# Optimization experiments

Hardware: AMD Instinct MI355X
Metric: run time of the kernel (lower is better)

The kernel has to match this reference:

```python
import jax, jax.numpy as jnp
import numpy as np

BN_EPS = 1e-5


def ball_query(pos, radius, k):
    """PointNet++-style ball query: for each point, the first k point indices
    (in index order) whose distance < radius; shorter lists are padded with the
    first valid index (self is always valid since dist=0). pos: (b,n,3).
    Returns idx: (b,n,k) int32."""
    b, n, _ = pos.shape
    sq = jnp.sum(pos * pos, axis=-1)                       # (b,n)
    d2 = sq[:, :, None] + sq[:, None, :] - 2.0 * jnp.einsum('bnc,bmc->bnm', pos, pos)
    mask = d2 < radius * radius                            # (b,n,n)
    cand = jnp.where(mask, jnp.arange(n, dtype=jnp.int32)[None, None, :], jnp.int32(n))
    # smallest-k indices in ascending order == first-k valid in index order
    neg_top, _ = jax.lax.top_k(-cand, k)                   # (b,n,k)
    idx = -neg_top
    first = idx[..., :1]
    idx = jnp.where(idx == n, first, idx)                  # pad with first neighbor
    return idx


def reference(pos, x, w1, gamma, beta, w2, b2, radius, k):
    pos = jax.lax.stop_gradient(pos)
    idx = ball_query(pos, radius, k)                       # (b,n,k)
    grouped = jax.vmap(lambda p, i: p[i])(pos, idx)        # (b,n,k,3)
    rel = grouped - pos[:, :, None, :]                     # center-subtract
    # 1x1 conv (3->3, no bias)
    h = jnp.einsum('bnkc,dc->bnkd', rel, w1)
    # BatchNorm2d (training-mode batch stats over b,k,n per channel)
    mean = jnp.mean(h, axis=(0, 1, 2))
    var = jnp.mean((h - mean) ** 2, axis=(0, 1, 2))
    h = (h - mean) * jax.lax.rsqrt(var + BN_EPS) * gamma + beta
    h = jax.nn.relu(h)
    # 1x1 conv (3->out_channel) + bias
    pe = jnp.einsum('bnkd,ed->bnke', h, w2) + b2           # (b,n,k,C)
    pe = jnp.max(pe, axis=2)                               # max over k neighbors
    return x + pe


def setup_inputs() -> dict:
    key = jax.random.key(0)
    ks = jax.random.split(key, 5)
    b, n, c, kk = 2, 8192, 64, 32
    pos = jax.random.uniform(ks[0], (b, n, 3), dtype=jnp.float32)
    x = jax.random.normal(ks[1], (b, n, c), dtype=jnp.float32)
    w1 = jax.random.normal(ks[2], (3, 3), dtype=jnp.float32) * 0.5
    gamma = jnp.ones((3,), dtype=jnp.float32)
    beta = jnp.zeros((3,), dtype=jnp.float32)
    w2 = jax.random.normal(ks[3], (c, 3), dtype=jnp.float32) * 0.5
    b2 = jnp.zeros((c,), dtype=jnp.float32)
    radius = jnp.float32(0.1)
    return {"pos": pos, "x": x, "w1": w1, "gamma": gamma, "beta": beta,
            "w2": w2, "b2": b2, "radius": radius, "k": kk}
```

## Files before the change

### kernel.cpp

```cpp
#include <hip/hip_runtime.h>
#include <math.h>

#define NPTS   8192
#define NBATCH 2
#define NQ     (NPTS * NBATCH)
#define KNB    32
#define CFEAT  64
#define BN_EPS 1e-5f

#define MAXC     1000
#define CSTR     1024
#define CAP_HIT  128

#define QBK2  4
#define NBLK2 (NQ / QBK2)

#define QBK3  16
#define NBLK3 (NQ / QBK3)

#define WS_H     0
#define WS_PART  (NQ * 3 * KNB)
#define WS_STATS (WS_PART + 6 * NBLK2)
#define WS_CS    (WS_STATS + 8)
#define WS_BIN   (WS_CS + 2 * CSTR)

__device__ __forceinline__ int grid_from_r(double rd) {
    int G = (int)(1.0 / rd);
    if (G < 1) G = 1;
    while (G > 1 && 1.0 / (double)G < rd) --G;
    if (G > 10) G = 10;
    return G;
}

__device__ __forceinline__ int mbcnt64(unsigned long long m) {
    return (int)__builtin_amdgcn_mbcnt_hi((unsigned)(m >> 32),
             __builtin_amdgcn_mbcnt_lo((unsigned)m, 0u));
}

__global__ __launch_bounds__(256) void kA_bin(
    const float* __restrict__ pos, const float* __restrict__ radius,
    float* __restrict__ ws)
{
    __shared__ int hist[MAXC];
    __shared__ int offs[MAXC];
    __shared__ int cur[MAXC];
    __shared__ int wtot[4];

    const int tid = threadIdx.x, lane = tid & 63, wave = tid >> 6;
    const int batch = blockIdx.x;
    const float* bpos = pos + (size_t)batch * NPTS * 3;
    const double rd = (double)radius[0];
    const int G = grid_from_r(rd);
    const float Gf = (float)G;
    const int NC = G * G * G;

    for (int c = tid; c < NC; c += 256) hist[c] = 0;
    __syncthreads();
    for (int p = tid; p < NPTS; p += 256) {
        float x = bpos[p * 3], y = bpos[p * 3 + 1], z = bpos[p * 3 + 2];
        int cx = min((int)(x * Gf), G - 1);
        int cy = min((int)(y * Gf), G - 1);
        int cz = min((int)(z * Gf), G - 1);
        atomicAdd(&hist[(cz * G + cy) * G + cx], 1);
    }
    __syncthreads();

    const int c0 = tid * 4;
    int h0 = (c0 + 0 < NC) ? hist[c0 + 0] : 0;
    int h1 = (c0 + 1 < NC) ? hist[c0 + 1] : 0;
    int h2 = (c0 + 2 < NC) ? hist[c0 + 2] : 0;
    int h3 = (c0 + 3 < NC) ? hist[c0 + 3] : 0;
    const int tsum = h0 + h1 + h2 + h3;
    int incl = tsum;
#pragma unroll
    for (int off = 1; off < 64; off <<= 1) {
        int v = __shfl_up(incl, off);
        if (lane >= off) incl += v;
    }
    if (lane == 63) wtot[wave] = incl;
    __syncthreads();
    int wbase = 0;
#pragma unroll
    for (int w = 0; w < 4; ++w) wbase += (w < wave) ? wtot[w] : 0;
    int base = wbase + incl - tsum;
    if (c0 + 0 < NC) { offs[c0 + 0] = base; cur[c0 + 0] = base; base += h0; }
    if (c0 + 1 < NC) { offs[c0 + 1] = base; cur[c0 + 1] = base; base += h1; }
    if (c0 + 2 < NC) { offs[c0 + 2] = base; cur[c0 + 2] = base; base += h2; }
    if (c0 + 3 < NC) { offs[c0 + 3] = base; cur[c0 + 3] = base; base += h3; }
    __syncthreads();

    int* cs = (int*)ws + WS_CS + batch * CSTR;
    for (int c = tid; c <= NC; c += 256) cs[c] = (c < NC) ? offs[c] : NPTS;

    float4* bin = (float4*)(ws + WS_BIN) + (size_t)batch * NPTS;
    for (int p = tid; p < NPTS; p += 256) {
        float x = bpos[p * 3], y = bpos[p * 3 + 1], z = bpos[p * 3 + 2];
        int cx = min((int)(x * Gf), G - 1);
        int cy = min((int)(y * Gf), G - 1);
        int cz = min((int)(z * Gf), G - 1);
        int slot = atomicAdd(&cur[(cz * G + cy) * G + cx], 1);
        bin[slot] = make_float4(x, y, z, __int_as_float(p));
    }
}

__global__ __launch_bounds__(256) void k2_query(
    const float* __restrict__ pos, const float* __restrict__ w1,
    const float* __restrict__ radius, float* __restrict__ ws)
{
    __shared__ int   hitl[QBK2][CAP_HIT];
    __shared__ int   seli[QBK2][KNB];
    __shared__ float sred[QBK2][6];

    const int tid = threadIdx.x, lane = tid & 63, wave = tid >> 6;
    const int qbase = blockIdx.x * QBK2;
    const int batch = qbase / NPTS;
    const float* bpos = pos + (size_t)batch * NPTS * 3;
    const double rd  = (double)radius[0];
    const double r2d = rd * rd;
    const int G = grid_from_r(rd);
    const float Gf = (float)G;
    const int* cs = (const int*)ws + WS_CS + batch * CSTR;
    const float4* bin = (const float4*)(ws + WS_BIN) + (size_t)batch * NPTS;

    const int qg = qbase + wave;
    const int ql = qg - batch * NPTS;
    const float qx = bpos[ql * 3], qy = bpos[ql * 3 + 1], qz = bpos[ql * 3 + 2];
    const double qxd = (double)qx, qyd = (double)qy, qzd = (double)qz;
    const double qsd = fma(qzd, qzd, fma(qyd, qyd, qxd * qxd));
    const int cx = min((int)(qx * Gf), G - 1);
    const int cy = min((int)(qy * Gf), G - 1);
    const int cz = min((int)(qz * Gf), G - 1);
    const int cx0 = max(cx - 1, 0), cx1 = min(cx + 1, G - 1);

    int hc = 0;
#pragma unroll
    for (int r = 0; r < 9; ++r) {
        const int ny = cy + (r % 3) - 1;
        const int nz = cz + (r / 3) - 1;
        if (ny < 0 || ny >= G || nz < 0 || nz >= G) continue;
        const int cb = (nz * G + ny) * G;
        const int s0 = cs[cb + cx0];
        const int s1 = cs[cb + cx1 + 1];
        for (int b0 = s0; b0 < s1; b0 += 64) {
            const int ss = b0 + lane;
            const bool act = ss < s1;
            float4 P = bin[act ? ss : s0];
            double xj = (double)P.x, yj = (double)P.y, zj = (double)P.z;
            double sqj = fma(zj, zj, fma(yj, yj, xj * xj));
            double dot = fma(zj, qzd, fma(yj, qyd, xj * qxd));
            double dd  = (qsd + sqj) - 2.0 * dot;
            bool in = act && (dd < r2d);
            unsigned long long bal = __ballot(in);
            if (in) {
                int p2 = hc + mbcnt64(bal);
                if (p2 < CAP_HIT) hitl[wave][p2] = __float_as_int(P.w);
            }
            hc += (int)__popcll(bal);
        }
    }
    if (hc > CAP_HIT) hc = CAP_HIT;

    if (hc <= KNB) {
        int v = (lane < hc) ? hitl[wave][lane] : 0x7FFFFFFF;
        int mn = v;
#pragma unroll
        for (int off = 32; off; off >>= 1) mn = min(mn, __shfl_xor(mn, off));
        if (lane < KNB) seli[wave][lane] = (lane < hc) ? v : mn;
    } else {
        int a = (lane < hc) ? hitl[wave][lane] : 0x7FFFFFFF;
        int b = (64 + lane < hc) ? hitl[wave][64 + lane] : 0x7FFFFFFF;
        int lo = 0, hi = NPTS - 1;
        while (lo < hi) {
            int mid = (lo + hi) >> 1;
            int c1 = (int)__popcll(__ballot(a <= mid)) +
                     (int)__popcll(__ballot(b <= mid));
            if (c1 >= KNB) hi = mid; else lo = mid + 1;
        }
        const int t = lo;
        unsigned long long ba = __ballot(a <= t);
        unsigned long long bb = __ballot(b <= t);
        int na = (int)__popcll(ba);
        if (a <= t) seli[wave][mbcnt64(ba)] = a;
        if (b <= t) seli[wave][na + mbcnt64(bb)] = b;
    }

    float w1r[9];
#pragma unroll
    for (int i = 0; i < 9; ++i) w1r[i] = w1[i];

    float ls0 = 0.f, ls1 = 0.f, ls2 = 0.f;
    float lq0 = 0.f, lq1 = 0.f, lq2 = 0.f;
    if (lane < KNB) {
        int j = seli[wave][lane];
        const float* pj = bpos + (size_t)j * 3;
        float rx = __fsub_rn(pj[0], qx);
        float ry = __fsub_rn(pj[1], qy);
        float rz = __fsub_rn(pj[2], qz);
        float h0 = fmaf(rz, w1r[2], fmaf(ry, w1r[1], __fmul_rn(rx, w1r[0])));
        float h1 = fmaf(rz, w1r[5], fmaf(ry, w1r[4], __fmul_rn(rx, w1r[3])));
        float h2 = fmaf(rz, w1r[8], fmaf(ry, w1r[7], __fmul_rn(rx, w1r[6])));
        float* hout = ws + WS_H + (size_t)qg * 3 * KNB;
        hout[0 * KNB + lane] = h0;
        hout[1 * KNB + lane] = h1;
        hout[2 * KNB + lane] = h2;
        ls0 = h0; ls1 = h1; ls2 = h2;
        lq0 = h0 * h0; lq1 = h1 * h1; lq2 = h2 * h2;
    }

#pragma unroll
    for (int m = 1; m < 64; m <<= 1) {
        ls0 += __shfl_xor(ls0, m); ls1 += __shfl_xor(ls1, m); ls2 += __shfl_xor(ls2, m);
        lq0 += __shfl_xor(lq0, m); lq1 += __shfl_xor(lq1, m); lq2 += __shfl_xor(lq2, m);
    }
    if (lane == 0) {
        sred[wave][0] = ls0; sred[wave][1] = ls1; sred[wave][2] = ls2;
        sred[wave][3] = lq0; sred[wave][4] = lq1; sred[wave][5] = lq2;
    }
    __syncthreads();
    if (tid < 6) {
        float s = sred[0][tid] + sred[1][tid] + sred[2][tid] + sred[3][tid];
        ws[WS_PART + tid * NBLK2 + blockIdx.x] = s;
    }
}

__global__ __launch_bounds__(1024) void k2b_stats(float* __restrict__ ws)
{
    __shared__ float wred[16][6];
    const int tid = threadIdx.x, lane = tid & 63, wave = tid >> 6;

#pragma unroll
    for (int c = 0; c < 6; ++c) {
        float s = 0.f;
        for (int i = tid; i < NBLK2; i += 1024) s += ws[WS_PART + c * NBLK2 + i];
#pragma unroll
        for (int m = 1; m < 64; m <<= 1) s += __shfl_xor(s, m);
        if (lane == 0) wred[wave][c] = s;
    }
    __syncthreads();
    if (tid < 3) {
        const double N = (double)((long long)NQ * KNB);
        double s = 0.0, sq = 0.0;
#pragma unroll
        for (int w = 0; w < 16; ++w) { s += wred[w][tid]; sq += wred[w][3 + tid]; }
        double mean = s / N;
        double var  = sq / N - mean * mean;
        ws[WS_STATS + tid]     = (float)mean;
        ws[WS_STATS + 3 + tid] = (float)(1.0 / sqrt(var + (double)BN_EPS));
    }
}

__global__ __launch_bounds__(256) void k3_mlp(
    const float* __restrict__ ws, const float* __restrict__ gamma,
    const float* __restrict__ beta, const float* __restrict__ w2,
    const float* __restrict__ b2, const float* __restrict__ x,
    float* __restrict__ out)
{
    __shared__ float gl[QBK3 * 96];

    const int tid = threadIdx.x;
    const float m0 = ws[WS_STATS + 0], m1 = ws[WS_STATS + 1], m2 = ws[WS_STATS + 2];
    const float i0 = ws[WS_STATS + 3], i1 = ws[WS_STATS + 4], i2 = ws[WS_STATS + 5];
    const float g0 = gamma[0], g1 = gamma[1], g2 = gamma[2];
    const float b0 = beta[0],  b1 = beta[1],  b2c = beta[2];

    const int qbase = blockIdx.x * QBK3;
    const float* hin = ws + WS_H + (size_t)qbase * 96;

#pragma unroll
    for (int r = 0; r < 6; ++r) {
        const int idx = r * 256 + tid;
        const int c = (idx % 96) >> 5;
        float h = hin[idx];
        float mm = c == 0 ? m0 : (c == 1 ? m1 : m2);
        float ii = c == 0 ? i0 : (c == 1 ? i1 : i2);
        float gg = c == 0 ? g0 : (c == 1 ? g1 : g2);
        float bb = c == 0 ? b0 : (c == 1 ? b1 : b2c);
        float n = __fadd_rn(__fmul_rn(__fmul_rn(__fsub_rn(h, mm), ii), gg), bb);
        gl[idx] = fmaxf(n, 0.0f);
    }
    __syncthreads();

    const int ch = tid & 63;
    const int qh = tid >> 6;
    const float w20 = w2[ch * 3 + 0];
    const float w21 = w2[ch * 3 + 1];
    const float w22 = w2[ch * 3 + 2];
    const float bias = b2[ch];

#pragma unroll
    for (int r = 0; r < 4; ++r) {
        const int q = r * 4 + qh;
        const float* gq = &gl[q * 96];
        float m = -INFINITY;
#pragma unroll 4
        for (int kk = 0; kk < KNB; ++kk) {
            float ga = gq[kk], gb = gq[32 + kk], gc = gq[64 + kk];
            float pe = __fadd_rn(fmaf(gc, w22, fmaf(gb, w21, __fmul_rn(ga, w20))), bias);
            m = fmaxf(m, pe);
        }
        const size_t o = (size_t)(qbase + q) * CFEAT + ch;
        out[o] = __fadd_rn(x[o], m);
    }
}

extern "C" void kernel_launch(void* const* d_in, const int* in_sizes, int n_in,
                              void* d_out, int out_size, void* d_ws, size_t ws_size,
                              hipStream_t stream) {
    (void)in_sizes; (void)n_in; (void)out_size; (void)ws_size;
    const float* pos    = (const float*)d_in[0];
    const float* x      = (const float*)d_in[1];
    const float* w1     = (const float*)d_in[2];
    const float* gamma  = (const float*)d_in[3];
    const float* beta   = (const float*)d_in[4];
    const float* w2     = (const float*)d_in[5];
    const float* b2     = (const float*)d_in[6];
    const float* radius = (const float*)d_in[7];
    float* out = (float*)d_out;
    float* ws  = (float*)d_ws;

    hipLaunchKernelGGL(kA_bin,    dim3(NBATCH), dim3(256),  0, stream, pos, radius, ws);
    hipLaunchKernelGGL(k2_query,  dim3(NBLK2),  dim3(256),  0, stream, pos, w1, radius, ws);
    hipLaunchKernelGGL(k2b_stats, dim3(1),      dim3(1024), 0, stream, ws);
    hipLaunchKernelGGL(k3_mlp,    dim3(NBLK3),  dim3(256),  0, stream,
                       ws, gamma, beta, w2, b2, x, out);
}
```

Baseline: 69.07 us.

## Parallelize spatial binning across blocks and flatten neighbor-cell scan in query

Replaces the two-block binning kernel with a memset, a grid-wide global-atomic histogram kernel, a single-block scan kernel and a grid-wide scatter kernel, so binning no longer runs serially on two workgroups. The query kernel now handles four queries per wave, which cuts the block count so the stats kernel reads exactly one partial per thread. It also concatenates the nine neighbor row ranges into one flat index space, so 64-lane loads are not wasted on short per-row tails. The cost is extra launches, contention on global atomics, and a nondeterministic point order within each cell, though the selection only depends on indices.

```diff
diff --git a/kernel.cpp b/kernel.cpp
--- a/kernel.cpp
+++ b/kernel.cpp
@@ -12,16 +12,18 @@
 #define CSTR     1024
 #define CAP_HIT  128
 
-#define QBK2  4
+#define QBK2  16
 #define NBLK2 (NQ / QBK2)
 
 #define QBK3  16
 #define NBLK3 (NQ / QBK3)
 
 #define WS_H     0
-#define WS_PART  (NQ * 3 * KNB)
+#define WS_PART  (WS_H + NQ * 3 * KNB)
 #define WS_STATS (WS_PART + 6 * NBLK2)
-#define WS_CS    (WS_STATS + 8)
+#define WS_HIST  (WS_STATS + 8)
+#define WS_CUR   (WS_HIST + 2 * CSTR)
+#define WS_CS    (WS_CUR + 2 * CSTR)
 #define WS_BIN   (WS_CS + 2 * CSTR)
 
 __device__ __forceinline__ int grid_from_r(double rd) {
@@ -37,79 +39,84 @@
              __builtin_amdgcn_mbcnt_lo((unsigned)m, 0u));
 }
 
-__global__ __launch_bounds__(256) void kA_bin(
+__device__ __forceinline__ int cell_of(float v, float Gf, int G) {
+    int c = (int)(v * Gf);
+    return c > G - 1 ? G - 1 : c;
+}
+
+__global__ __launch_bounds__(256) void kH_hist(
     const float* __restrict__ pos, const float* __restrict__ radius,
     float* __restrict__ ws)
 {
-    __shared__ int hist[MAXC];
-    __shared__ int offs[MAXC];
-    __shared__ int cur[MAXC];
-    __shared__ int wtot[4];
-
-    const int tid = threadIdx.x, lane = tid & 63, wave = tid >> 6;
-    const int batch = blockIdx.x;
-    const float* bpos = pos + (size_t)batch * NPTS * 3;
+    const int p = blockIdx.x * 256 + threadIdx.x;
+    const int batch = p >> 13;
+    const int pl = p & (NPTS - 1);
     const double rd = (double)radius[0];
     const int G = grid_from_r(rd);
     const float Gf = (float)G;
+    const float* pp = pos + (size_t)batch * NPTS * 3 + (size_t)pl * 3;
+    float x = pp[0], y = pp[1], z = pp[2];
+    int c = (cell_of(z, Gf, G) * G + cell_of(y, Gf, G)) * G + cell_of(x, Gf, G);
+    atomicAdd((int*)ws + WS_HIST + batch * CSTR + c, 1);
+}
+
+__global__ __launch_bounds__(1024) void kS_scan(
+    const float* __restrict__ radius, float* __restrict__ ws)
+{
+    __shared__ int wtot[16];
+    const int tid = threadIdx.x, lane = tid & 63, wave = tid >> 6;
+    const double rd = (double)radius[0];
+    const int G = grid_from_r(rd);
     const int NC = G * G * G;
 
-    for (int c = tid; c < NC; c += 256) hist[c] = 0;
-    __syncthreads();
-    for (int p = tid; p < NPTS; p += 256) {
-        float x = bpos[p * 3], y = bpos[p * 3 + 1], z = bpos[p * 3 + 2];
-        int cx = min((int)(x * Gf), G - 1);
-        int cy = min((int)(y * Gf), G - 1);
-        int cz = min((int)(z * Gf), G - 1);
-        atomicAdd(&hist[(cz * G + cy) * G + cx], 1);
-    }
-    __syncthreads();
-
-    const int c0 = tid * 4;
-    int h0 = (c0 + 0 < NC) ? hist[c0 + 0] : 0;
-    int h1 = (c0 + 1 < NC) ? hist[c0 + 1] : 0;
-    int h2 = (c0 + 2 < NC) ? hist[c0 + 2] : 0;
-    int h3 = (c0 + 3 < NC) ? hist[c0 + 3] : 0;
-    const int tsum = h0 + h1 + h2 + h3;
-    int incl = tsum;
-#pragma unroll
-    for (int off = 1; off < 64; off <<= 1) {
-        int v = __shfl_up(incl, off);
-        if (lane >= off) incl += v;
-    }
-    if (lane == 63) wtot[wave] = incl;
-    __syncthreads();
-    int wbase = 0;
-#pragma unroll
-    for (int w = 0; w < 4; ++w) wbase += (w < wave) ? wtot[w] : 0;
-    int base = wbase + incl - tsum;
-    if (c0 + 0 < NC) { offs[c0 + 0] = base; cur[c0 + 0] = base; base += h0; }
-    if (c0 + 1 < NC) { offs[c0 + 1] = base; cur[c0 + 1] = base; base += h1; }
-    if (c0 + 2 < NC) { offs[c0 + 2] = base; cur[c0 + 2] = base; base += h2; }
-    if (c0 + 3 < NC) { offs[c0 + 3] = base; cur[c0 + 3] = base; base += h3; }
-    __syncthreads();
-
-    int* cs = (int*)ws + WS_CS + batch * CSTR;
-    for (int c = tid; c <= NC; c += 256) cs[c] = (c < NC) ? offs[c] : NPTS;
-
+    for (int batch = 0; batch < NBATCH; ++batch) {
+        const int* hist = (const int*)ws + WS_HIST + batch * CSTR;
+        int* cur = (int*)ws + WS_CUR + batch * CSTR;
+        int* cs  = (int*)ws + WS_CS  + batch * CSTR;
+        int v = (tid < NC) ? hist[tid] : 0;
+        int incl = v;
+#pragma unroll
+        for (int off = 1; off < 64; off <<= 1) {
+            int t = __shfl_up(incl, off);
+            if (lane >= off) incl += t;
+        }
+        if (lane == 63) wtot[wave] = incl;
+        __syncthreads();
+        int base = 0;
+#pragma unroll
+        for (int w = 0; w < 16; ++w) base += (w < wave) ? wtot[w] : 0;
+        int excl = base + incl - v;
+        if (tid < NC) { cs[tid] = excl; cur[tid] = excl; }
+        if (tid == 0) cs[NC] = NPTS;
+        __syncthreads();
+    }
+}
+
+__global__ __launch_bounds__(256) void kC_scatter(
+    const float* __restrict__ pos, const float* __restrict__ radius,
+    float* __restrict__ ws)
+{
+    const int p = blockIdx.x * 256 + threadIdx.x;
+    const int batch = p >> 13;
+    const int pl = p & (NPTS - 1);
+    const double rd = (double)radius[0];
+    const int G = grid_from_r(rd);
+    const float Gf = (float)G;
+    const float* pp = pos + (size_t)batch * NPTS * 3 + (size_t)pl * 3;
+    float x = pp[0], y = pp[1], z = pp[2];
+    int c = (cell_of(z, Gf, G) * G + cell_of(y, Gf, G)) * G + cell_of(x, Gf, G);
+    int slot = atomicAdd((int*)ws + WS_CUR + batch * CSTR + c, 1);
     float4* bin = (float4*)(ws + WS_BIN) + (size_t)batch * NPTS;
-    for (int p = tid; p < NPTS; p += 256) {
-        float x = bpos[p * 3], y = bpos[p * 3 + 1], z = bpos[p * 3 + 2];
-        int cx = min((int)(x * Gf), G - 1);
-        int cy = min((int)(y * Gf), G - 1);
-        int cz = min((int)(z * Gf), G - 1);
-        int slot = atomicAdd(&cur[(cz * G + cy) * G + cx], 1);
-        bin[slot] = make_float4(x, y, z, __int_as_float(p));
-    }
+    bin[slot] = make_float4(x, y, z, __int_as_float(pl));
 }
 
 __global__ __launch_bounds__(256) void k2_query(
     const float* __restrict__ pos, const float* __restrict__ w1,
     const float* __restrict__ radius, float* __restrict__ ws)
 {
-    __shared__ int   hitl[QBK2][CAP_HIT];
-    __shared__ int   seli[QBK2][KNB];
-    __shared__ float sred[QBK2][6];
+    __shared__ int   hitl[4][CAP_HIT];
+    __shared__ int   seli[4][KNB];
+    __shared__ float sred[4][6];
 
     const int tid = threadIdx.x, lane = tid & 63, wave = tid >> 6;
     const int qbase = blockIdx.x * QBK2;
@@ -122,29 +129,51 @@
     const int* cs = (const int*)ws + WS_CS + batch * CSTR;
     const float4* bin = (const float4*)(ws + WS_BIN) + (size_t)batch * NPTS;
 
-    const int qg = qbase + wave;
-    const int ql = qg - batch * NPTS;
-    const float qx = bpos[ql * 3], qy = bpos[ql * 3 + 1], qz = bpos[ql * 3 + 2];
-    const double qxd = (double)qx, qyd = (double)qy, qzd = (double)qz;
-    const double qsd = fma(qzd, qzd, fma(qyd, qyd, qxd * qxd));
-    const int cx = min((int)(qx * Gf), G - 1);
-    const int cy = min((int)(qy * Gf), G - 1);
-    const int cz = min((int)(qz * Gf), G - 1);
-    const int cx0 = max(cx - 1, 0), cx1 = min(cx + 1, G - 1);
-
-    int hc = 0;
-#pragma unroll
-    for (int r = 0; r < 9; ++r) {
-        const int ny = cy + (r % 3) - 1;
-        const int nz = cz + (r / 3) - 1;
-        if (ny < 0 || ny >= G || nz < 0 || nz >= G) continue;
-        const int cb = (nz * G + ny) * G;
-        const int s0 = cs[cb + cx0];
-        const int s1 = cs[cb + cx1 + 1];
-        for (int b0 = s0; b0 < s1; b0 += 64) {
-            const int ss = b0 + lane;
-            const bool act = ss < s1;
-            float4 P = bin[act ? ss : s0];
+    float w1r[9];
+#pragma unroll
+    for (int i = 0; i < 9; ++i) w1r[i] = w1[i];
+
+    float ls0 = 0.f, ls1 = 0.f, ls2 = 0.f;
+    float lq0 = 0.f, lq1 = 0.f, lq2 = 0.f;
+
+#pragma unroll 1
+    for (int qq = 0; qq < 4; ++qq) {
+        const int qg = qbase + wave * 4 + qq;
+        const int ql = qg - batch * NPTS;
+        const float qx = bpos[ql * 3], qy = bpos[ql * 3 + 1], qz = bpos[ql * 3 + 2];
+        const double qxd = (double)qx, qyd = (double)qy, qzd = (double)qz;
+        const double qsd = fma(qzd, qzd, fma(qyd, qyd, qxd * qxd));
+        const int cx = cell_of(qx, Gf, G);
+        const int cy = cell_of(qy, Gf, G);
+        const int cz = cell_of(qz, Gf, G);
+        const int cx0 = max(cx - 1, 0), cx1 = min(cx + 1, G - 1);
+
+        int rs0[9], rpref[10];
+        int tot = 0;
+#pragma unroll
+        for (int r = 0; r < 9; ++r) {
+            const int ny = cy + (r % 3) - 1;
+            const int nz = cz + (r / 3) - 1;
+            int s0 = 0, len = 0;
+            if (ny >= 0 && ny < G && nz >= 0 && nz < G) {
+                const int cb = (nz * G + ny) * G;
+                s0  = cs[cb + cx0];
+                len = cs[cb + cx1 + 1] - s0;
+            }
+            rs0[r] = s0; rpref[r] = tot; tot += len;
+        }
+        rpref[9] = tot;
+
+        int hc = 0;
+        for (int b0 = 0; b0 < tot; b0 += 64) {
+            const int flat = b0 + lane;
+            const bool act = flat < tot;
+            int ss = flat + (rs0[0] - rpref[0]);
+#pragma unroll
+            for (int i = 1; i < 9; ++i)
+                ss += (flat >= rpref[i]) ? ((rs0[i] - rpref[i]) -
+                                            (rs0[i - 1] - rpref[i - 1])) : 0;
+            float4 P = bin[act ? ss : 0];
             double xj = (double)P.x, yj = (double)P.y, zj = (double)P.z;
             double sqj = fma(zj, zj, fma(yj, yj, xj * xj));
             double dot = fma(zj, qzd, fma(yj, qyd, xj * qxd));
@@ -157,54 +186,48 @@
             }
             hc += (int)__popcll(bal);
         }
-    }
-    if (hc > CAP_HIT) hc = CAP_HIT;
-
-    if (hc <= KNB) {
-        int v = (lane < hc) ? hitl[wave][lane] : 0x7FFFFFFF;
-        int mn = v;
-#pragma unroll
-        for (int off = 32; off; off >>= 1) mn = min(mn, __shfl_xor(mn, off));
-        if (lane < KNB) seli[wave][lane] = (lane < hc) ? v : mn;
-    } else {
-        int a = (lane < hc) ? hitl[wave][lane] : 0x7FFFFFFF;
-        int b = (64 + lane < hc) ? hitl[wave][64 + lane] : 0x7FFFFFFF;
-        int lo = 0, hi = NPTS - 1;
-        while (lo < hi) {
-            int mid = (lo + hi) >> 1;
-            int c1 = (int)__popcll(__ballot(a <= mid)) +
-                     (int)__popcll(__ballot(b <= mid));
-            if (c1 >= KNB) hi = mid; else lo = mid + 1;
-        }
-        const int t = lo;
-        unsigned long long ba = __ballot(a <= t);
-        unsigned long long bb = __ballot(b <= t);
-        int na = (int)__popcll(ba);
-        if (a <= t) seli[wave][mbcnt64(ba)] = a;
-        if (b <= t) seli[wave][na + mbcnt64(bb)] = b;
-    }
-
-    float w1r[9];
-#pragma unroll
-    for (int i = 0; i < 9; ++i) w1r[i] = w1[i];
-
-    float ls0 = 0.f, ls1 = 0.f, ls2 = 0.f;
-    float lq0 = 0.f, lq1 = 0.f, lq2 = 0.f;
-    if (lane < KNB) {
-        int j = seli[wave][lane];
-        const float* pj = bpos + (size_t)j * 3;
-        float rx = __fsub_rn(pj[0], qx);
-        float ry = __fsub_rn(pj[1], qy);
-        float rz = __fsub_rn(pj[2], qz);
-        float h0 = fmaf(rz, w1r[2], fmaf(ry, w1r[1], __fmul_rn(rx, w1r[0])));
-        float h1 = fmaf(rz, w1r[5], fmaf(ry, w1r[4], __fmul_rn(rx, w1r[3])));
-        float h2 = fmaf(rz, w1r[8], fmaf(ry, w1r[7], __fmul_rn(rx, w1r[6])));
-        float* hout = ws + WS_H + (size_t)qg * 3 * KNB;
-        hout[0 * KNB + lane] = h0;
-        hout[1 * KNB + lane] = h1;
-        hout[2 * KNB + lane] = h2;
-        ls0 = h0; ls1 = h1; ls2 = h2;
-        lq0 = h0 * h0; lq1 = h1 * h1; lq2 = h2 * h2;
+        if (hc > CAP_HIT) hc = CAP_HIT;
+
+        if (hc <= KNB) {
+            int v = (lane < hc) ? hitl[wave][lane] : 0x7FFFFFFF;
+            int mn = v;
+#pragma unroll
+            for (int off = 32; off; off >>= 1) mn = min(mn, __shfl_xor(mn, off));
+            if (lane < KNB) seli[wave][lane] = (lane < hc) ? v : mn;
+        } else {
+            int a = (lane < hc) ? hitl[wave][lane] : 0x7FFFFFFF;
+            int b = (64 + lane < hc) ? hitl[wave][64 + lane] : 0x7FFFFFFF;
+            int lo = 0, hi = NPTS - 1;
+            while (lo < hi) {
+                int mid = (lo + hi) >> 1;
+                int c1 = (int)__popcll(__ballot(a <= mid)) +
+                         (int)__popcll(__ballot(b <= mid));
+                if (c1 >= KNB) hi = mid; else lo = mid + 1;
+            }
+            const int t = lo;
+            unsigned long long ba = __ballot(a <= t);
+            unsigned long long bb = __ballot(b <= t);
+            int na = (int)__popcll(ba);
+            if (a <= t) seli[wave][mbcnt64(ba)] = a;
+            if (b <= t) seli[wave][na + mbcnt64(bb)] = b;
+        }
+
+        if (lane < KNB) {
+            int j = seli[wave][lane];
+            const float* pj = bpos + (size_t)j * 3;
+            float rx = __fsub_rn(pj[0], qx);
+            float ry = __fsub_rn(pj[1], qy);
+            float rz = __fsub_rn(pj[2], qz);
+            float h0 = fmaf(rz, w1r[2], fmaf(ry, w1r[1], __fmul_rn(rx, w1r[0])));
+            float h1 = fmaf(rz, w1r[5], fmaf(ry, w1r[4], __fmul_rn(rx, w1r[3])));
+            float h2 = fmaf(rz, w1r[8], fmaf(ry, w1r[7], __fmul_rn(rx, w1r[6])));
+            float* hout = ws + WS_H + (size_t)qg * 3 * KNB;
+            hout[0 * KNB + lane] = h0;
+            hout[1 * KNB + lane] = h1;
+            hout[2 * KNB + lane] = h2;
+            ls0 += h0; ls1 += h1; ls2 += h2;
+            lq0 += h0 * h0; lq1 += h1 * h1; lq2 += h2 * h2;
+        }
     }
 
 #pragma unroll
@@ -230,8 +253,7 @@
 
 #pragma unroll
     for (int c = 0; c < 6; ++c) {
-        float s = 0.f;
-        for (int i = tid; i < NBLK2; i += 1024) s += ws[WS_PART + c * NBLK2 + i];
+        float s = ws[WS_PART + c * NBLK2 + tid];
 #pragma unroll
         for (int m = 1; m < 64; m <<= 1) s += __shfl_xor(s, m);
         if (lane == 0) wred[wave][c] = s;
@@ -318,9 +340,12 @@
     float* out = (float*)d_out;
     float* ws  = (float*)d_ws;
 
-    hipLaunchKernelGGL(kA_bin,    dim3(NBATCH), dim3(256),  0, stream, pos, radius, ws);
-    hipLaunchKernelGGL(k2_query,  dim3(NBLK2),  dim3(256),  0, stream, pos, w1, radius, ws);
-    hipLaunchKernelGGL(k2b_stats, dim3(1),      dim3(1024), 0, stream, ws);
-    hipLaunchKernelGGL(k3_mlp,    dim3(NBLK3),  dim3(256),  0, stream,
+    hipMemsetAsync(ws + WS_HIST, 0, 2 * CSTR * sizeof(int), stream);
+    hipLaunchKernelGGL(kH_hist,    dim3(NQ / 256), dim3(256),  0, stream, pos, radius, ws);
+    hipLaunchKernelGGL(kS_scan,    dim3(1),        dim3(1024), 0, stream, radius, ws);
+    hipLaunchKernelGGL(kC_scatter, dim3(NQ / 256), dim3(256),  0, stream, pos, radius, ws);
+    hipLaunchKernelGGL(k2_query,   dim3(NBLK2),    dim3(256),  0, stream, pos, w1, radius, ws);
+    hipLaunchKernelGGL(k2b_stats,  dim3(1),        dim3(1024), 0, stream, ws);
+    hipLaunchKernelGGL(k3_mlp,     dim3(NBLK3),    dim3(256),  0, stream,
                        ws, gamma, beta, w2, b2, x, out);
 }
```

After: 66.03 us. -4.4%, faster.
